# Optimization experiments

Hardware: AMD Instinct MI355X
Metric: run time of the kernel (lower is better)

The kernel has to match this reference:

```python
import jax, jax.numpy as jnp
import numpy as np

N_NODES = 50000
N_EDGES = 800000
ORIG_FEA = 92
NBR_FEA = 41
HID = 64
N_CONV = 3
BN_EPS = 1e-5


def setup_inputs() -> dict:
    key = jax.random.key(0)
    ks = jax.random.split(key, 16)
    s = 0.05
    inp = {
        "x": jax.random.normal(ks[0], (N_NODES, ORIG_FEA), dtype=jnp.float32),
        "edge_attr": jax.random.normal(ks[1], (N_EDGES, NBR_FEA), dtype=jnp.float32),
        "edge_index": jax.random.randint(ks[2], (2, N_EDGES), 0, N_NODES, dtype=jnp.int64),
        # embedding1 / embedding2
        "W1": jax.random.normal(ks[3], (ORIG_FEA, HID), dtype=jnp.float32) * s,
        "b1": jnp.zeros((HID,), dtype=jnp.float32),
        "W2": jax.random.normal(ks[4], (NBR_FEA, HID), dtype=jnp.float32) * s,
        "b2": jnp.zeros((HID,), dtype=jnp.float32),
        # CGConv lin_f / lin_s per layer, stacked [n_conv, 3*HID, HID]
        "Wf": jax.random.normal(ks[5], (N_CONV, 3 * HID, HID), dtype=jnp.float32) * s,
        "bf": jnp.zeros((N_CONV, HID), dtype=jnp.float32),
        "Ws": jax.random.normal(ks[6], (N_CONV, 3 * HID, HID), dtype=jnp.float32) * s,
        "bs": jnp.zeros((N_CONV, HID), dtype=jnp.float32),
        # BatchNorm1d per layer (training mode: batch statistics)
        "gamma": jnp.ones((N_CONV, HID), dtype=jnp.float32),
        "beta": jnp.zeros((N_CONV, HID), dtype=jnp.float32),
    }
    return inp


def _cgconv(x, e, src, tgt, Wf, bf, Ws, bs):
    # z_ij = [x_i (target), x_j (source), e_ij]  -> [E, 3H]
    z = jnp.concatenate([x[tgt], x[src], e], axis=-1)
    gate = jax.nn.sigmoid(z @ Wf + bf)
    core = jax.nn.softplus(z @ Ws + bs)
    msg = gate * core  # [E, H]
    agg = jax.ops.segment_sum(msg, tgt, num_segments=x.shape[0])
    return x + agg  # residual


def _batchnorm(x, gamma, beta):
    mean = jnp.mean(x, axis=0)
    var = jnp.mean(jnp.square(x - mean), axis=0)  # biased var (torch BN training)
    return (x - mean) * jax.lax.rsqrt(var + BN_EPS) * gamma + beta


def reference(x, edge_attr, edge_index, W1, b1, W2, b2, Wf, bf, Ws, bs, gamma, beta):
    src, tgt = edge_index[0], edge_index[1]
    h = x @ W1 + b1                 # embedding1: [N, H]
    e = edge_attr @ W2 + b2         # embedding2: [E, H]
    for i in range(N_CONV):
        h = _cgconv(h, e, src, tgt, Wf[i], bf[i], Ws[i], bs[i])
        h = _batchnorm(h, gamma[i], beta[i])
        if i < N_CONV - 1:
            h = jax.nn.relu(h)
        # drop_ratio = 0 -> dropout is identity
    return h
```

## Files before the change

kernel.cpp:

```cpp
#include <hip/hip_runtime.h>
#include <cmath>

#define NNODES 50000
#define NEDGES 800000
#define ORIG_FEA 92
#define NBR_FEA 41
#define HID 64
#define BN_EPS 1e-5f
#define ECOLS 48

typedef __attribute__((ext_vector_type(8))) short short8;
typedef __attribute__((ext_vector_type(4))) float f32x4;
typedef unsigned short ushort;
typedef unsigned int uint;

static __device__ __forceinline__ ushort f2bf(float f) {
    uint u = __float_as_uint(f);
    uint r = u + 0x7fffu + ((u >> 16) & 1u);
    return (ushort)(r >> 16);
}

#define EMBED_BASE 221
#define EMBED_BLOCKS 1024

__global__ __launch_bounds__(256) void prep_embed(
    const float* __restrict__ W2, const float* __restrict__ b2,
    const float* __restrict__ Wf, const float* __restrict__ bf,
    const float* __restrict__ Ws, const float* __restrict__ bs,
    ushort* __restrict__ Bpack, ushort* __restrict__ Tpack,
    float* __restrict__ bcf, float* __restrict__ bcs,
    float* __restrict__ stats, int* __restrict__ deg,
    const float* __restrict__ x, const float* __restrict__ W1,
    const float* __restrict__ b1, float* __restrict__ h,
    ushort* __restrict__ h_bf) {
    if (blockIdx.x >= EMBED_BASE) {
        int lane = threadIdx.x & 63;
        int wid = (((int)blockIdx.x - EMBED_BASE) * 256 + (int)threadIdx.x) >> 6;
        int nw = (EMBED_BLOCKS * 256) >> 6;
        float b1v = b1[lane];
        for (int n = wid; n < NNODES; n += nw) {
            const float* xr = x + (long)n * ORIG_FEA;
            float xa = xr[lane];
            float xb = (lane < ORIG_FEA - 64) ? xr[64 + lane] : 0.f;
            float a0 = b1v, a1 = 0.f, a2 = 0.f, a3 = 0.f;
            #pragma unroll
            for (int k = 0; k < 64; k += 4) {
                a0 = fmaf(__shfl(xa, k, 64),     W1[k * HID + lane], a0);
                a1 = fmaf(__shfl(xa, k + 1, 64), W1[(k + 1) * HID + lane], a1);
                a2 = fmaf(__shfl(xa, k + 2, 64), W1[(k + 2) * HID + lane], a2);
                a3 = fmaf(__shfl(xa, k + 3, 64), W1[(k + 3) * HID + lane], a3);
            }
            #pragma unroll
            for (int k = 0; k < ORIG_FEA - 64; k += 4) {
                a0 = fmaf(__shfl(xb, k, 64),     W1[(64 + k) * HID + lane], a0);
                a1 = fmaf(__shfl(xb, k + 1, 64), W1[(65 + k) * HID + lane], a1);
                a2 = fmaf(__shfl(xb, k + 2, 64), W1[(66 + k) * HID + lane], a2);
                a3 = fmaf(__shfl(xb, k + 3, 64), W1[(67 + k) * HID + lane], a3);
            }
            float acc = (a0 + a1) + (a2 + a3);
            h[(long)n * HID + lane] = acc;
            h_bf[(long)n * HID + lane] = f2bf(acc);
        }
        return;
    }
    if (blockIdx.x >= 25) {
        int i = ((int)blockIdx.x - 25) * 256 + (int)threadIdx.x;
        if (i < NNODES) deg[i] = 0;
        return;
    }
    if (blockIdx.x == 24) {
        for (int i = threadIdx.x; i < 3 * 128; i += blockDim.x) stats[i] = 0.f;
        return;
    }
    int group = blockIdx.x >> 2;
    int quarter = blockIdx.x & 3;
    int layer = group >> 1;
    int fs = group & 1;
    const float* Wbig = (fs ? Ws : Wf) + layer * 192 * HID;
    const float* We = Wbig + 128 * HID;
    const float* bvec = (fs ? bs : bf) + layer * HID;
    float* bc = (fs ? bcs : bcf) + layer * HID;
    ushort* Bp = Bpack + layer * 16384 + fs * 8192;
    ushort* Tp = Tpack + layer * 8192 + fs * 4096;

    for (int idx = quarter * 2048 + threadIdx.x; idx < (quarter + 1) * 2048;
         idx += blockDim.x) {
        int j = idx & 7;
        int lane = (idx >> 3) & 63;
        int ck = (idx >> 9) & 3;
        int tt = (idx >> 11) & 3;
        int k = ck * 32 + ((lane >> 4) * 8) + j;
        int col = tt * 16 + (lane & 15);
        float v = 0.f;
        if (k < 64) v = Wbig[(64 + k) * HID + col];
        else if (k < 64 + NBR_FEA) {
            int r = k - 64;
            float a = 0.f;
            for (int m = 0; m < HID; ++m) a += W2[r * HID + m] * We[m * HID + col];
            v = a;
        }
        Bp[(tt * 4 + ck) * 512 + lane * 8 + j] = f2bf(v);
    }
    for (int idx = quarter * 1024 + threadIdx.x; idx < (quarter + 1) * 1024;
         idx += blockDim.x) {
        int j = idx & 7;
        int lane = (idx >> 3) & 63;
        int ck = (idx >> 9) & 1;
        int t = (idx >> 10) & 3;
        int k = ck * 32 + ((lane >> 4) * 8) + j;
        int col = t * 16 + (lane & 15);
        Tp[(t * 2 + ck) * 512 + lane * 8 + j] = f2bf(Wbig[k * HID + col]);
    }
    if (quarter == 3) {
        for (int c0 = threadIdx.x; c0 < HID; c0 += blockDim.x) {
            float a = bvec[c0];
            for (int m = 0; m < HID; ++m) a += b2[m] * We[m * HID + c0];
            bc[c0] = a;
        }
    }
}

__global__ void k_hist(const int* __restrict__ eidx, int* __restrict__ deg) {
    int e = blockIdx.x * blockDim.x + threadIdx.x;
    if (e < NEDGES) atomicAdd(&deg[eidx[NEDGES + e]], 1);
}

__global__ void k_blocksum(const int* __restrict__ deg, int* __restrict__ bsum) {
    __shared__ int sh[256];
    int i = blockIdx.x * 256 + threadIdx.x;
    sh[threadIdx.x] = (i < NNODES) ? deg[i] : 0;
    __syncthreads();
    for (int s = 128; s > 0; s >>= 1) {
        if (threadIdx.x < s) sh[threadIdx.x] += sh[threadIdx.x + s];
        __syncthreads();
    }
    if (threadIdx.x == 0) bsum[blockIdx.x] = sh[0];
}

__global__ void k_scanbase(const int* __restrict__ bsum, int* __restrict__ bbase,
                           int* __restrict__ rowptr) {
    __shared__ int sh[256];
    int t = threadIdx.x;
    int v = (t < 196) ? bsum[t] : 0;
    sh[t] = v;
    __syncthreads();
    for (int s = 1; s < 256; s <<= 1) {
        int add = (t >= s) ? sh[t - s] : 0;
        __syncthreads();
        sh[t] += add;
        __syncthreads();
    }
    if (t < 196) bbase[t] = sh[t] - v;
    if (t == 0) rowptr[NNODES] = NEDGES;
}

__global__ void k_writerow(const int* __restrict__ deg, const int* __restrict__ bbase,
                           int* __restrict__ rowptr, int* __restrict__ cursor) {
    __shared__ int sh[256];
    int t = threadIdx.x;
    int i = blockIdx.x * 256 + t;
    int v = (i < NNODES) ? deg[i] : 0;
    sh[t] = v;
    __syncthreads();
    for (int s = 1; s < 256; s <<= 1) {
        int add = (t >= s) ? sh[t - s] : 0;
        __syncthreads();
        sh[t] += add;
        __syncthreads();
    }
    if (i < NNODES) {
        int e = bbase[blockIdx.x] + sh[t] - v;
        rowptr[i] = e;
        cursor[i] = e;
    }
}

__global__ __launch_bounds__(256) void scatterA_eab(
    const int* __restrict__ eidx, int* __restrict__ cursor,
    int* __restrict__ srcs, const float* __restrict__ ea,
    ushort* __restrict__ eab_s) {
    int e = blockIdx.x * blockDim.x + threadIdx.x;
    if (e >= NEDGES) return;
    const float* row = ea + (long)e * NBR_FEA;
    float a[NBR_FEA];
    #pragma unroll
    for (int k = 0; k < NBR_FEA; ++k) a[k] = row[k];
    int tgt = eidx[NEDGES + e];
    int pos = atomicAdd(&cursor[tgt], 1);
    srcs[pos] = eidx[e];
    uint u[24];
    #pragma unroll
    for (int m = 0; m < 20; ++m)
        u[m] = (uint)f2bf(a[2 * m]) | ((uint)f2bf(a[2 * m + 1]) << 16);
    u[20] = (uint)f2bf(a[40]);
    u[21] = 0u; u[22] = 0u; u[23] = 0u;
    uint4* dst = (uint4*)(eab_s + (long)pos * ECOLS);
    #pragma unroll
    for (int m = 0; m < 6; ++m) {
        uint4 o; o.x = u[4 * m]; o.y = u[4 * m + 1];
        o.z = u[4 * m + 2]; o.w = u[4 * m + 3];
        dst[m] = o;
    }
}

__global__ __launch_bounds__(256) void proj_mfma(
    const ushort* __restrict__ h_bf, const ushort* __restrict__ Tpack_l,
    const float* __restrict__ bcf_l, const float* __restrict__ bcs_l,
    float* __restrict__ Ttgt) {
    int lane = threadIdx.x & 63;
    int cc = lane & 15;
    int g = lane >> 4;
    short8 Bf[4][2], Bs[4][2];
    #pragma unroll
    for (int t = 0; t < 4; ++t)
        #pragma unroll
        for (int ck = 0; ck < 2; ++ck) {
            Bf[t][ck] = *(const short8*)(Tpack_l + (t * 2 + ck) * 512 + lane * 8);
            Bs[t][ck] = *(const short8*)(Tpack_l + 4096 + (t * 2 + ck) * 512 + lane * 8);
        }
    float bfv[4], bsv[4];
    #pragma unroll
    for (int t = 0; t < 4; ++t) {
        bfv[t] = bcf_l[t * 16 + cc];
        bsv[t] = bcs_l[t * 16 + cc];
    }
    int wid = (blockIdx.x * blockDim.x + threadIdx.x) >> 6;
    int nw = (gridDim.x * blockDim.x) >> 6;
    for (int nb = wid; nb < NNODES / 16; nb += nw) {
        long base = (long)nb * 16;
        long row = base + cc;
        short8 A0 = *(const short8*)(h_bf + row * 64 + g * 8);
        short8 A1 = *(const short8*)(h_bf + row * 64 + 32 + g * 8);
        f32x4 accf[4], accs[4];
        f32x4 z4 = {0.f, 0.f, 0.f, 0.f};
        #pragma unroll
        for (int t = 0; t < 4; ++t) {
            accf[t] = __builtin_amdgcn_mfma_f32_16x16x32_bf16(A0, Bf[t][0], z4, 0, 0, 0);
            accs[t] = __builtin_amdgcn_mfma_f32_16x16x32_bf16(A0, Bs[t][0], z4, 0, 0, 0);
        }
        #pragma unroll
        for (int t = 0; t < 4; ++t) {
            accf[t] = __builtin_amdgcn_mfma_f32_16x16x32_bf16(A1, Bf[t][1], accf[t], 0, 0, 0);
            accs[t] = __builtin_amdgcn_mfma_f32_16x16x32_bf16(A1, Bs[t][1], accs[t], 0, 0, 0);
        }
        #pragma unroll
        for (int r = 0; r < 4; ++r) {
            long node = base + g * 4 + r;
            f32x4 vf = {accf[0][r] + bfv[0], accf[1][r] + bfv[1],
                        accf[2][r] + bfv[2], accf[3][r] + bfv[3]};
            f32x4 vs = {accs[0][r] + bsv[0], accs[1][r] + bsv[1],
                        accs[2][r] + bsv[2], accs[3][r] + bsv[3]};
            *(f32x4*)(Ttgt + node * 128 + cc * 4) = vf;
            *(f32x4*)(Ttgt + node * 128 + 64 + cc * 4) = vs;
        }
    }
}

__global__ __launch_bounds__(256, 2) void edge_kernel(
    const ushort* __restrict__ eab_s, const int* __restrict__ srcs,
    const int* __restrict__ rowptr, const ushort* __restrict__ h_bf,
    const float* __restrict__ h, const float* __restrict__ Ttgt,
    const ushort* __restrict__ Bpack, float* __restrict__ agg,
    float* __restrict__ stats) {
    int lane = threadIdx.x & 63;
    int q = lane >> 4;
    int c = lane & 15;
    int wid = (blockIdx.x * blockDim.x + threadIdx.x) >> 6;
    int nw = (gridDim.x * blockDim.x) >> 6;
    const short8 z8 = {0, 0, 0, 0, 0, 0, 0, 0};

    short8 B[8][4];
    #pragma unroll
    for (int t = 0; t < 8; ++t)
        #pragma unroll
        for (int ck = 0; ck < 4; ++ck)
            B[t][ck] = *(const short8*)(Bpack + ((t * 4 + ck) * 512 + lane * 8));

    float st1 = 0.f, st2 = 0.f;
    int tn = wid;
    int r0 = 0, r1 = 0, svAll = 0;
    short8 A0, A1, A2, A3;
    if (tn < NNODES) {
        r0 = rowptr[tn]; r1 = rowptr[tn + 1];
        int e = r0 + lane; if (e > NEDGES - 1) e = NEDGES - 1;
        svAll = srcs[e];
        int sv = __shfl(svAll, c, 64);
        int ei = r0 + c; if (ei > NEDGES - 1) ei = NEDGES - 1;
        const short8* hrow = (const short8*)(h_bf + (long)sv * 64);
        const ushort* erow = eab_s + (long)ei * ECOLS;
        A0 = hrow[q]; A1 = hrow[4 + q];
        A2 = *(const short8*)(erow + q * 8);
        A3 = z8;
        if (q < 2) A3 = *(const short8*)(erow + 32 + q * 8);
    }

    while (tn < NNODES) {
        int tn2 = tn + nw;
        int r0n = 0, r1n = 0;
        if (tn2 < NNODES) { r0n = rowptr[tn2]; r1n = rowptr[tn2 + 1]; }
        f32x4 tf = *(const f32x4*)(Ttgt + (long)tn * 128 + 4 * c);
        f32x4 ts = *(const f32x4*)(Ttgt + (long)tn * 128 + 64 + 4 * c);
        int d = r1 - r0;
        int nch = (d + 15) >> 4;
        float vs0 = 0.f, vs1 = 0.f, vs2 = 0.f, vs3 = 0.f;

        if (nch == 0) {
            int e = r0n + lane; if (e > NEDGES - 1) e = NEDGES - 1;
            svAll = srcs[e];
            int sv = __shfl(svAll, c, 64);
            int ei = r0n + c; if (ei > NEDGES - 1) ei = NEDGES - 1;
            const short8* hrow = (const short8*)(h_bf + (long)sv * 64);
            const ushort* erow = eab_s + (long)ei * ECOLS;
            A0 = hrow[q]; A1 = hrow[4 + q];
            A2 = *(const short8*)(erow + q * 8);
            A3 = z8;
            if (q < 2) A3 = *(const short8*)(erow + 32 + q * 8);
        } else {
            for (int ci = 0; ci < nch; ++ci) {
                int sv, ei;
                int nidx = ci + 1;
                if (nidx < nch) {
                    if ((nidx & 3) == 0) {
                        int e = r0 + nidx * 16 + lane;
                        if (e > NEDGES - 1) e = NEDGES - 1;
                        svAll = srcs[e];
                    }
                    sv = __shfl(svAll, ((nidx & 3) << 4) + c, 64);
                    ei = r0 + nidx * 16 + c;
                    if (ei > NEDGES - 1) ei = NEDGES - 1;
                } else {
                    int e = r0n + lane; if (e > NEDGES - 1) e = NEDGES - 1;
                    svAll = srcs[e];
                    sv = __shfl(svAll, c, 64);
                    ei = r0n + c; if (ei > NEDGES - 1) ei = NEDGES - 1;
                }
                const short8* hrow = (const short8*)(h_bf + (long)sv * 64);
                const ushort* erow = eab_s + (long)ei * ECOLS;
                short8 N0 = hrow[q], N1 = hrow[4 + q];
                short8 N2 = *(const short8*)(erow + q * 8);
                short8 N3 = z8;
                if (q < 2) N3 = *(const short8*)(erow + 32 + q * 8);

                f32x4 accf[4], accs[4];
                f32x4 z4 = {0.f, 0.f, 0.f, 0.f};
                __builtin_amdgcn_s_setprio(1);
                #pragma unroll
                for (int t = 0; t < 4; ++t) {
                    accf[t] = __builtin_amdgcn_mfma_f32_16x16x32_bf16(A0, B[t][0], z4, 0, 0, 0);
                    accs[t] = __builtin_amdgcn_mfma_f32_16x16x32_bf16(A0, B[t + 4][0], z4, 0, 0, 0);
                }
                #pragma unroll
                for (int t = 0; t < 4; ++t) {
                    accf[t] = __builtin_amdgcn_mfma_f32_16x16x32_bf16(A1, B[t][1], accf[t], 0, 0, 0);
                    accs[t] = __builtin_amdgcn_mfma_f32_16x16x32_bf16(A1, B[t + 4][1], accs[t], 0, 0, 0);
                }
                #pragma unroll
                for (int t = 0; t < 4; ++t) {
                    accf[t] = __builtin_amdgcn_mfma_f32_16x16x32_bf16(A2, B[t][2], accf[t], 0, 0, 0);
                    accs[t] = __builtin_amdgcn_mfma_f32_16x16x32_bf16(A2, B[t + 4][2], accs[t], 0, 0, 0);
                }
                #pragma unroll
                for (int t = 0; t < 4; ++t) {
                    accf[t] = __builtin_amdgcn_mfma_f32_16x16x32_bf16(A3, B[t][3], accf[t], 0, 0, 0);
                    accs[t] = __builtin_amdgcn_mfma_f32_16x16x32_bf16(A3, B[t + 4][3], accs[t], 0, 0, 0);
                }
                __builtin_amdgcn_s_setprio(0);

                int base = ci * 16 + q * 4;
                #pragma unroll
                for (int r = 0; r < 4; ++r) {
                    bool valid = (base + r) < d;
                    #pragma unroll
                    for (int t = 0; t < 4; ++t) {
                        float f = accf[t][r] + tf[t];
                        float s = accs[t][r] + ts[t];
                        float g = __builtin_amdgcn_rcpf(1.f + __expf(-f));
                        float sp = fmaxf(s, 0.f) + __logf(1.f + __expf(-fabsf(s)));
                        float msg = valid ? g * sp : 0.f;
                        if (t == 0) vs0 += msg;
                        else if (t == 1) vs1 += msg;
                        else if (t == 2) vs2 += msg;
                        else vs3 += msg;
                    }
                }
                A0 = N0; A1 = N1; A2 = N2; A3 = N3;
            }
        }
        vs0 += __shfl_xor(vs0, 16, 64); vs0 += __shfl_xor(vs0, 32, 64);
        vs1 += __shfl_xor(vs1, 16, 64); vs1 += __shfl_xor(vs1, 32, 64);
        vs2 += __shfl_xor(vs2, 16, 64); vs2 += __shfl_xor(vs2, 32, 64);
        vs3 += __shfl_xor(vs3, 16, 64); vs3 += __shfl_xor(vs3, 32, 64);
        float out = (q == 0) ? vs0 : (q == 1) ? vs1 : (q == 2) ? vs2 : vs3;
        agg[(long)tn * 64 + lane] = out;
        float v = h[(long)tn * 64 + lane] + out;
        st1 += v;
        st2 = fmaf(v, v, st2);

        tn = tn2; r0 = r0n; r1 = r1n;
    }

    __shared__ float ls[4][64], lq[4][64];
    int w = threadIdx.x >> 6;
    ls[w][lane] = st1; lq[w][lane] = st2;
    __syncthreads();
    if (threadIdx.x < 64) {
        float t1 = ls[0][lane] + ls[1][lane] + ls[2][lane] + ls[3][lane];
        float t2 = lq[0][lane] + lq[1][lane] + lq[2][lane] + lq[3][lane];
        atomicAdd(&stats[lane], t1);
        atomicAdd(&stats[64 + lane], t2);
    }
}

__global__ __launch_bounds__(256) void bnproj(
    float* __restrict__ h, const float* __restrict__ agg,
    const float* __restrict__ stats, const float* __restrict__ gamma,
    const float* __restrict__ beta, ushort* __restrict__ h_bf,
    const ushort* __restrict__ Tpack_l, const float* __restrict__ bcf_l,
    const float* __restrict__ bcs_l, float* __restrict__ Ttgt) {
    int lane = threadIdx.x & 63;
    int cc = lane & 15;
    int g = lane >> 4;
    short8 Bf[4][2], Bs[4][2];
    #pragma unroll
    for (int t = 0; t < 4; ++t)
        #pragma unroll
        for (int ck = 0; ck < 2; ++ck) {
            Bf[t][ck] = *(const short8*)(Tpack_l + (t * 2 + ck) * 512 + lane * 8);
            Bs[t][ck] = *(const short8*)(Tpack_l + 4096 + (t * 2 + ck) * 512 + lane * 8);
        }
    float bfv[4], bsv[4];
    #pragma unroll
    for (int t = 0; t < 4; ++t) {
        bfv[t] = bcf_l[t * 16 + cc];
        bsv[t] = bcs_l[t * 16 + cc];
    }
    const float invn = 1.f / (float)NNODES;
    float sc[16], sh[16];
    #pragma unroll
    for (int m = 0; m < 16; ++m) {
        int ch = (m < 8) ? (g * 8 + m) : (32 + g * 8 + (m - 8));
        float mu = stats[ch] * invn;
        float va = stats[64 + ch] * invn - mu * mu;
        float s = rsqrtf(va + BN_EPS) * gamma[ch];
        sc[m] = s;
        sh[m] = beta[ch] - mu * s;
    }
    int wid = (blockIdx.x * blockDim.x + threadIdx.x) >> 6;
    int nw = (gridDim.x * blockDim.x) >> 6;
    for (int nb = wid; nb < NNODES / 16; nb += nw) {
        long base = (long)nb * 16;
        long row = base + cc;
        float* hr = h + row * 64;
        const float* ar = agg + row * 64;
        float y[16];
        #pragma unroll
        for (int half = 0; half < 2; ++half) {
            int col = half * 32 + g * 8;
            f32x4 hv0 = *(const f32x4*)(hr + col);
            f32x4 hv1 = *(const f32x4*)(hr + col + 4);
            f32x4 av0 = *(const f32x4*)(ar + col);
            f32x4 av1 = *(const f32x4*)(ar + col + 4);
            #pragma unroll
            for (int m = 0; m < 4; ++m) {
                float t0 = (hv0[m] + av0[m]) * sc[half * 8 + m] + sh[half * 8 + m];
                float t1 = (hv1[m] + av1[m]) * sc[half * 8 + 4 + m] + sh[half * 8 + 4 + m];
                y[half * 8 + m] = fmaxf(t0, 0.f);
                y[half * 8 + 4 + m] = fmaxf(t1, 0.f);
            }
        }
        f32x4 w0 = {y[0], y[1], y[2], y[3]},   w1 = {y[4], y[5], y[6], y[7]};
        f32x4 w2 = {y[8], y[9], y[10], y[11]}, w3 = {y[12], y[13], y[14], y[15]};
        *(f32x4*)(hr + g * 8) = w0;       *(f32x4*)(hr + g * 8 + 4) = w1;
        *(f32x4*)(hr + 32 + g * 8) = w2;  *(f32x4*)(hr + 32 + g * 8 + 4) = w3;
        uint u[8];
        #pragma unroll
        for (int m = 0; m < 8; ++m)
            u[m] = (uint)f2bf(y[m * 2]) | ((uint)f2bf(y[m * 2 + 1]) << 16);
        uint4 p0; p0.x = u[0]; p0.y = u[1]; p0.z = u[2]; p0.w = u[3];
        uint4 p1; p1.x = u[4]; p1.y = u[5]; p1.z = u[6]; p1.w = u[7];
        *(uint4*)(h_bf + row * 64 + g * 8) = p0;
        *(uint4*)(h_bf + row * 64 + 32 + g * 8) = p1;
        short8 A0 = *reinterpret_cast<short8*>(&p0);
        short8 A1 = *reinterpret_cast<short8*>(&p1);

        f32x4 accf[4], accs[4];
        f32x4 z4 = {0.f, 0.f, 0.f, 0.f};
        #pragma unroll
        for (int t = 0; t < 4; ++t) {
            accf[t] = __builtin_amdgcn_mfma_f32_16x16x32_bf16(A0, Bf[t][0], z4, 0, 0, 0);
            accs[t] = __builtin_amdgcn_mfma_f32_16x16x32_bf16(A0, Bs[t][0], z4, 0, 0, 0);
        }
        #pragma unroll
        for (int t = 0; t < 4; ++t) {
            accf[t] = __builtin_amdgcn_mfma_f32_16x16x32_bf16(A1, Bf[t][1], accf[t], 0, 0, 0);
            accs[t] = __builtin_amdgcn_mfma_f32_16x16x32_bf16(A1, Bs[t][1], accs[t], 0, 0, 0);
        }
        #pragma unroll
        for (int r = 0; r < 4; ++r) {
            long node = base + g * 4 + r;
            f32x4 vf = {accf[0][r] + bfv[0], accf[1][r] + bfv[1],
                        accf[2][r] + bfv[2], accf[3][r] + bfv[3]};
            f32x4 vs = {accs[0][r] + bsv[0], accs[1][r] + bsv[1],
                        accs[2][r] + bsv[2], accs[3][r] + bsv[3]};
            *(f32x4*)(Ttgt + node * 128 + cc * 4) = vf;
            *(f32x4*)(Ttgt + node * 128 + 64 + cc * 4) = vs;
        }
    }
}

__global__ __launch_bounds__(256) void bn_final(
    float* __restrict__ h, const float* __restrict__ agg,
    const float* __restrict__ stats, const float* __restrict__ gamma,
    const float* __restrict__ beta) {
    int tid = blockIdx.x * blockDim.x + threadIdx.x;
    int nth = gridDim.x * blockDim.x;
    const float invn = 1.f / (float)NNODES;
    int cb = (tid & 15) * 4;
    f32x4 sc, sh;
    #pragma unroll
    for (int j = 0; j < 4; ++j) {
        float m = stats[cb + j] * invn;
        float v = stats[64 + cb + j] * invn - m * m;
        float s = rsqrtf(v + BN_EPS) * gamma[cb + j];
        sc[j] = s;
        sh[j] = beta[cb + j] - m * s;
    }
    for (long i = tid; i < (long)NNODES * 16; i += nth) {
        f32x4 v = ((const f32x4*)h)[i];
        f32x4 a = ((const f32x4*)agg)[i];
        f32x4 y;
        #pragma unroll
        for (int j = 0; j < 4; ++j) y[j] = (v[j] + a[j]) * sc[j] + sh[j];
        ((f32x4*)h)[i] = y;
    }
}

extern "C" void kernel_launch(void* const* d_in, const int* in_sizes, int n_in,
                              void* d_out, int out_size, void* d_ws, size_t ws_size,
                              hipStream_t stream) {
    const float* x    = (const float*)d_in[0];
    const float* ea   = (const float*)d_in[1];
    const int*   eidx = (const int*)d_in[2];
    const float* W1   = (const float*)d_in[3];
    const float* b1   = (const float*)d_in[4];
    const float* W2   = (const float*)d_in[5];
    const float* b2   = (const float*)d_in[6];
    const float* Wf   = (const float*)d_in[7];
    const float* bf   = (const float*)d_in[8];
    const float* Ws   = (const float*)d_in[9];
    const float* bs   = (const float*)d_in[10];
    const float* gamma= (const float*)d_in[11];
    const float* beta = (const float*)d_in[12];
    float* h = (float*)d_out;

    char* wb = (char*)d_ws;
    auto align = [&]() { wb = (char*)(((size_t)wb + 255) & ~(size_t)255); };
    ushort* Bpack = (ushort*)wb;  wb += 3 * 8 * 4 * 512 * sizeof(ushort); align();
    ushort* Tpack = (ushort*)wb;  wb += 3 * 2 * 4 * 2 * 512 * sizeof(ushort); align();
    float* bcf   = (float*)wb;    wb += 3 * HID * sizeof(float);
    float* bcs   = (float*)wb;    wb += 3 * HID * sizeof(float);
    float* stats = (float*)wb;    wb += 3 * 2 * HID * sizeof(float); align();
    int* deg     = (int*)wb;      wb += NNODES * sizeof(int);
    int* rowptr  = (int*)wb;      wb += (NNODES + 1) * sizeof(int);
    int* cursor  = (int*)wb;      wb += NNODES * sizeof(int);
    int* bsum    = (int*)wb;      wb += 256 * sizeof(int);
    int* bbase   = (int*)wb;      wb += 256 * sizeof(int); align();
    int* srcs    = (int*)wb;      wb += NEDGES * sizeof(int);
    align();
    float* Ttgt  = (float*)wb;    wb += (size_t)NNODES * 128 * sizeof(float);
    float* agg   = (float*)wb;    wb += (size_t)NNODES * HID * sizeof(float);
    ushort* h_bf = (ushort*)wb;   wb += (size_t)NNODES * HID * sizeof(ushort);
    ushort* eab_s= (ushort*)wb;   wb += (size_t)NEDGES * ECOLS * sizeof(ushort);

    prep_embed<<<EMBED_BASE + EMBED_BLOCKS, 256, 0, stream>>>(
        W2, b2, Wf, bf, Ws, bs, Bpack, Tpack, bcf, bcs, stats, deg,
        x, W1, b1, h, h_bf);
    k_hist<<<(NEDGES + 255) / 256, 256, 0, stream>>>(eidx, deg);
    k_blocksum<<<196, 256, 0, stream>>>(deg, bsum);
    k_scanbase<<<1, 256, 0, stream>>>(bsum, bbase, rowptr);
    k_writerow<<<196, 256, 0, stream>>>(deg, bbase, rowptr, cursor);
    scatterA_eab<<<(NEDGES + 255) / 256, 256, 0, stream>>>(eidx, cursor, srcs,
                                                           ea, eab_s);
    proj_mfma<<<1024, 256, 0, stream>>>(h_bf, Tpack, bcf, bcs, Ttgt);

    for (int i = 0; i < 3; ++i) {
        edge_kernel<<<2048, 256, 0, stream>>>(eab_s, srcs, rowptr, h_bf, h, Ttgt,
                                              Bpack + i * 16384, agg, stats + i * 128);
        if (i < 2)
            bnproj<<<1024, 256, 0, stream>>>(h, agg, stats + i * 128, gamma + i * HID,
                                             beta + i * HID, h_bf,
                                             Tpack + (i + 1) * 8192,
                                             bcf + (i + 1) * HID, bcs + (i + 1) * HID,
                                             Ttgt);
        else
            bn_final<<<2048, 256, 0, stream>>>(h, agg, stats + i * 128,
                                               gamma + i * HID, beta + i * HID);
    }
}
```

Before: 765.4 us.

## Fuse histogram into prep and scatter into projection, stage edge weights in LDS

The degree histogram now runs inside the prep/embedding launch, with deg cleared by a memset beforehand. The edge scatter and the first node projection are merged into one launch so the two independent jobs overlap. The edge kernel reads its packed B weights from a 32KB shared-memory copy instead of holding them in registers, and its launch bound moves from 2 to 4 blocks per CU to raise occupancy. In exchange, every MFMA operand becomes an LDS read and each block pays to load the weights at startup.

```diff
diff --git a/kernel.cpp b/kernel.cpp
--- a/kernel.cpp
+++ b/kernel.cpp
@@ -20,7 +20,9 @@
     return (ushort)(r >> 16);
 }
 
-#define EMBED_BASE 221
+#define HIST_BASE 25
+#define HIST_BLOCKS 3125
+#define EMBED_BASE (HIST_BASE + HIST_BLOCKS)
 #define EMBED_BLOCKS 1024
 
 __global__ __launch_bounds__(256) void prep_embed(
@@ -30,6 +32,7 @@
     ushort* __restrict__ Bpack, ushort* __restrict__ Tpack,
     float* __restrict__ bcf, float* __restrict__ bcs,
     float* __restrict__ stats, int* __restrict__ deg,
+    const int* __restrict__ eidx,
     const float* __restrict__ x, const float* __restrict__ W1,
     const float* __restrict__ b1, float* __restrict__ h,
     ushort* __restrict__ h_bf) {
@@ -63,9 +66,9 @@
         }
         return;
     }
-    if (blockIdx.x >= 25) {
-        int i = ((int)blockIdx.x - 25) * 256 + (int)threadIdx.x;
-        if (i < NNODES) deg[i] = 0;
+    if (blockIdx.x >= HIST_BASE) {
+        int e = ((int)blockIdx.x - HIST_BASE) * 256 + (int)threadIdx.x;
+        if (e < NEDGES) atomicAdd(&deg[eidx[NEDGES + e]], 1);
         return;
     }
     if (blockIdx.x == 24) {
@@ -120,11 +123,6 @@
     }
 }
 
-__global__ void k_hist(const int* __restrict__ eidx, int* __restrict__ deg) {
-    int e = blockIdx.x * blockDim.x + threadIdx.x;
-    if (e < NEDGES) atomicAdd(&deg[eidx[NEDGES + e]], 1);
-}
-
 __global__ void k_blocksum(const int* __restrict__ deg, int* __restrict__ bsum) {
     __shared__ int sh[256];
     int i = blockIdx.x * 256 + threadIdx.x;
@@ -175,38 +173,41 @@
     }
 }
 
-__global__ __launch_bounds__(256) void scatterA_eab(
+#define SCAT_BLOCKS 3125
+#define PROJ_BLOCKS 1024
+
+__global__ __launch_bounds__(256) void scat_proj(
     const int* __restrict__ eidx, int* __restrict__ cursor,
     int* __restrict__ srcs, const float* __restrict__ ea,
-    ushort* __restrict__ eab_s) {
-    int e = blockIdx.x * blockDim.x + threadIdx.x;
-    if (e >= NEDGES) return;
-    const float* row = ea + (long)e * NBR_FEA;
-    float a[NBR_FEA];
-    #pragma unroll
-    for (int k = 0; k < NBR_FEA; ++k) a[k] = row[k];
-    int tgt = eidx[NEDGES + e];
-    int pos = atomicAdd(&cursor[tgt], 1);
-    srcs[pos] = eidx[e];
-    uint u[24];
-    #pragma unroll
-    for (int m = 0; m < 20; ++m)
-        u[m] = (uint)f2bf(a[2 * m]) | ((uint)f2bf(a[2 * m + 1]) << 16);
-    u[20] = (uint)f2bf(a[40]);
-    u[21] = 0u; u[22] = 0u; u[23] = 0u;
-    uint4* dst = (uint4*)(eab_s + (long)pos * ECOLS);
-    #pragma unroll
-    for (int m = 0; m < 6; ++m) {
-        uint4 o; o.x = u[4 * m]; o.y = u[4 * m + 1];
-        o.z = u[4 * m + 2]; o.w = u[4 * m + 3];
-        dst[m] = o;
-    }
-}
-
-__global__ __launch_bounds__(256) void proj_mfma(
+    ushort* __restrict__ eab_s,
     const ushort* __restrict__ h_bf, const ushort* __restrict__ Tpack_l,
     const float* __restrict__ bcf_l, const float* __restrict__ bcs_l,
     float* __restrict__ Ttgt) {
+    if (blockIdx.x < SCAT_BLOCKS) {
+        int e = blockIdx.x * 256 + threadIdx.x;
+        if (e >= NEDGES) return;
+        const float* row = ea + (long)e * NBR_FEA;
+        float a[NBR_FEA];
+        #pragma unroll
+        for (int k = 0; k < NBR_FEA; ++k) a[k] = row[k];
+        int tgt = eidx[NEDGES + e];
+        int pos = atomicAdd(&cursor[tgt], 1);
+        srcs[pos] = eidx[e];
+        uint u[24];
+        #pragma unroll
+        for (int m = 0; m < 20; ++m)
+            u[m] = (uint)f2bf(a[2 * m]) | ((uint)f2bf(a[2 * m + 1]) << 16);
+        u[20] = (uint)f2bf(a[40]);
+        u[21] = 0u; u[22] = 0u; u[23] = 0u;
+        uint4* dst = (uint4*)(eab_s + (long)pos * ECOLS);
+        #pragma unroll
+        for (int m = 0; m < 6; ++m) {
+            uint4 o; o.x = u[4 * m]; o.y = u[4 * m + 1];
+            o.z = u[4 * m + 2]; o.w = u[4 * m + 3];
+            dst[m] = o;
+        }
+        return;
+    }
     int lane = threadIdx.x & 63;
     int cc = lane & 15;
     int g = lane >> 4;
@@ -224,8 +225,8 @@
         bfv[t] = bcf_l[t * 16 + cc];
         bsv[t] = bcs_l[t * 16 + cc];
     }
-    int wid = (blockIdx.x * blockDim.x + threadIdx.x) >> 6;
-    int nw = (gridDim.x * blockDim.x) >> 6;
+    int wid = (((int)blockIdx.x - SCAT_BLOCKS) * 256 + (int)threadIdx.x) >> 6;
+    int nw = (PROJ_BLOCKS * 256) >> 6;
     for (int nb = wid; nb < NNODES / 16; nb += nw) {
         long base = (long)nb * 16;
         long row = base + cc;
@@ -256,25 +257,26 @@
     }
 }
 
-__global__ __launch_bounds__(256, 2) void edge_kernel(
+#define BL(t, ck) (*(const short8*)(Bl + (((t) * 4 + (ck)) * 512 + lane * 8)))
+
+__global__ __launch_bounds__(256, 4) void edge_kernel(
     const ushort* __restrict__ eab_s, const int* __restrict__ srcs,
     const int* __restrict__ rowptr, const ushort* __restrict__ h_bf,
     const float* __restrict__ h, const float* __restrict__ Ttgt,
     const ushort* __restrict__ Bpack, float* __restrict__ agg,
     float* __restrict__ stats) {
+    __shared__ ushort Bl[16384];
+    __shared__ float ls[4][64], lq[4][64];
+    for (int i = threadIdx.x; i < 2048; i += 256)
+        ((uint4*)Bl)[i] = ((const uint4*)Bpack)[i];
+    __syncthreads();
+
     int lane = threadIdx.x & 63;
     int q = lane >> 4;
     int c = lane & 15;
     int wid = (blockIdx.x * blockDim.x + threadIdx.x) >> 6;
     int nw = (gridDim.x * blockDim.x) >> 6;
     const short8 z8 = {0, 0, 0, 0, 0, 0, 0, 0};
-
-    short8 B[8][4];
-    #pragma unroll
-    for (int t = 0; t < 8; ++t)
-        #pragma unroll
-        for (int ck = 0; ck < 4; ++ck)
-            B[t][ck] = *(const short8*)(Bpack + ((t * 4 + ck) * 512 + lane * 8));
 
     float st1 = 0.f, st2 = 0.f;
     int tn = wid;
@@ -346,23 +348,23 @@
                 __builtin_amdgcn_s_setprio(1);
                 #pragma unroll
                 for (int t = 0; t < 4; ++t) {
-                    accf[t] = __builtin_amdgcn_mfma_f32_16x16x32_bf16(A0, B[t][0], z4, 0, 0, 0);
-                    accs[t] = __builtin_amdgcn_mfma_f32_16x16x32_bf16(A0, B[t + 4][0], z4, 0, 0, 0);
+                    accf[t] = __builtin_amdgcn_mfma_f32_16x16x32_bf16(A0, BL(t, 0), z4, 0, 0, 0);
+                    accs[t] = __builtin_amdgcn_mfma_f32_16x16x32_bf16(A0, BL(t + 4, 0), z4, 0, 0, 0);
                 }
                 #pragma unroll
                 for (int t = 0; t < 4; ++t) {
-                    accf[t] = __builtin_amdgcn_mfma_f32_16x16x32_bf16(A1, B[t][1], accf[t], 0, 0, 0);
-                    accs[t] = __builtin_amdgcn_mfma_f32_16x16x32_bf16(A1, B[t + 4][1], accs[t], 0, 0, 0);
+                    accf[t] = __builtin_amdgcn_mfma_f32_16x16x32_bf16(A1, BL(t, 1), accf[t], 0, 0, 0);
+                    accs[t] = __builtin_amdgcn_mfma_f32_16x16x32_bf16(A1, BL(t + 4, 1), accs[t], 0, 0, 0);
                 }
                 #pragma unroll
                 for (int t = 0; t < 4; ++t) {
-                    accf[t] = __builtin_amdgcn_mfma_f32_16x16x32_bf16(A2, B[t][2], accf[t], 0, 0, 0);
-                    accs[t] = __builtin_amdgcn_mfma_f32_16x16x32_bf16(A2, B[t + 4][2], accs[t], 0, 0, 0);
+                    accf[t] = __builtin_amdgcn_mfma_f32_16x16x32_bf16(A2, BL(t, 2), accf[t], 0, 0, 0);
+                    accs[t] = __builtin_amdgcn_mfma_f32_16x16x32_bf16(A2, BL(t + 4, 2), accs[t], 0, 0, 0);
                 }
                 #pragma unroll
                 for (int t = 0; t < 4; ++t) {
-                    accf[t] = __builtin_amdgcn_mfma_f32_16x16x32_bf16(A3, B[t][3], accf[t], 0, 0, 0);
-                    accs[t] = __builtin_amdgcn_mfma_f32_16x16x32_bf16(A3, B[t + 4][3], accs[t], 0, 0, 0);
+                    accf[t] = __builtin_amdgcn_mfma_f32_16x16x32_bf16(A3, BL(t, 3), accf[t], 0, 0, 0);
+                    accs[t] = __builtin_amdgcn_mfma_f32_16x16x32_bf16(A3, BL(t + 4, 3), accs[t], 0, 0, 0);
                 }
                 __builtin_amdgcn_s_setprio(0);
 
@@ -399,7 +401,6 @@
         tn = tn2; r0 = r0n; r1 = r1n;
     }
 
-    __shared__ float ls[4][64], lq[4][64];
     int w = threadIdx.x >> 6;
     ls[w][lane] = st1; lq[w][lane] = st2;
     __syncthreads();
@@ -572,16 +573,15 @@
     ushort* h_bf = (ushort*)wb;   wb += (size_t)NNODES * HID * sizeof(ushort);
     ushort* eab_s= (ushort*)wb;   wb += (size_t)NEDGES * ECOLS * sizeof(ushort);
 
+    hipMemsetAsync(deg, 0, NNODES * sizeof(int), stream);
     prep_embed<<<EMBED_BASE + EMBED_BLOCKS, 256, 0, stream>>>(
-        W2, b2, Wf, bf, Ws, bs, Bpack, Tpack, bcf, bcs, stats, deg,
+        W2, b2, Wf, bf, Ws, bs, Bpack, Tpack, bcf, bcs, stats, deg, eidx,
         x, W1, b1, h, h_bf);
-    k_hist<<<(NEDGES + 255) / 256, 256, 0, stream>>>(eidx, deg);
     k_blocksum<<<196, 256, 0, stream>>>(deg, bsum);
     k_scanbase<<<1, 256, 0, stream>>>(bsum, bbase, rowptr);
     k_writerow<<<196, 256, 0, stream>>>(deg, bbase, rowptr, cursor);
-    scatterA_eab<<<(NEDGES + 255) / 256, 256, 0, stream>>>(eidx, cursor, srcs,
-                                                           ea, eab_s);
-    proj_mfma<<<1024, 256, 0, stream>>>(h_bf, Tpack, bcf, bcs, Ttgt);
+    scat_proj<<<SCAT_BLOCKS + PROJ_BLOCKS, 256, 0, stream>>>(
+        eidx, cursor, srcs, ea, eab_s, h_bf, Tpack, bcf, bcs, Ttgt);
 
     for (int i = 0; i < 3; ++i) {
         edge_kernel<<<2048, 256, 0, stream>>>(eab_s, srcs, rowptr, h_bf, h, Ttgt,
```

After: 2.116 ms. 176% more time.
